# Performance work log

Measured on AMD Instinct MI355X. Metric: run time of the kernel, lower is better.

Reference implementation:

```python
import jax, jax.numpy as jnp
import numpy as np

B, S, D, H = 32, 8192, 256, 256


def setup_inputs() -> dict:
    key = jax.random.key(0)
    ks = jax.random.split(key, 8)
    # start token: module uses np.random.seed(42); np.random.random([B,1,D])
    rng = np.random.RandomState(42)
    start_token = jnp.asarray(rng.random_sample((B, 1, D)).astype(np.float32))
    s = 0.05  # weight init scale
    return {
        "encoder_output": jax.random.normal(ks[0], (B, S, D), jnp.float32),
        "h0": jax.random.normal(ks[1], (B, H), jnp.float32),
        "c0": jax.random.normal(ks[2], (B, H), jnp.float32),
        "start_token": start_token,
        # Keras LSTM params: kernel [D,4H], recurrent_kernel [H,4H], bias [4H]; gate order i,f,c,o
        "W_k": jax.random.normal(ks[3], (D, 4 * H), jnp.float32) * s,
        "W_r": jax.random.normal(ks[4], (H, 4 * H), jnp.float32) * s,
        "b_lstm": jnp.zeros((4 * H,), jnp.float32),
        # encoder_weight Dense(H), decode_weight Dense(H), v Dense(1)
        "W_e": jax.random.normal(ks[5], (D, H), jnp.float32) * s,
        "b_e": jnp.zeros((H,), jnp.float32),
        "W_d": jax.random.normal(ks[6], (H, H), jnp.float32) * s,
        "b_d": jnp.zeros((H,), jnp.float32),
        "v_w": jax.random.normal(ks[7], (H, 1), jnp.float32) * s,
        "v_b": jnp.zeros((1,), jnp.float32),
    }


def reference(encoder_output, h0, c0, start_token, W_k, W_r, b_lstm,
              W_e, b_e, W_d, b_d, v_w, v_b):
    # --- one Keras-LSTM step on the start token (seq_len = 1) ---
    x = start_token[:, 0, :]                      # [B, D]
    z = x @ W_k + h0 @ W_r + b_lstm               # [B, 4H]
    i, f, g, o = jnp.split(z, 4, axis=-1)         # Keras gate order i,f,c,o
    c = jax.nn.sigmoid(f) * c0 + jax.nn.sigmoid(i) * jnp.tanh(g)
    h = jax.nn.sigmoid(o) * jnp.tanh(c)           # [B, H] decoder output
    # --- Bahdanau additive attention (vectorized form of the double loop) ---
    dec_proj = h @ W_d + b_d                      # [B, H]
    enc_proj = encoder_output @ W_e + b_e         # [B, S, H]
    # tanh(enc_proj + dec_proj) projected to scalar by v
    scores = jnp.tanh(enc_proj + dec_proj[:, None, :]) @ v_w  # [B, S, 1]
    scores = scores[..., 0] + v_b                 # [B, S]
    return jax.nn.softmax(scores, axis=-1)
```

## Files before the change

kernel.cpp:

```cpp
#include <hip/hip_runtime.h>
#include <hip/hip_bf16.h>
#include <stdint.h>

#define B 32
#define S 8192
#define D 256
#define H 256

typedef __attribute__((ext_vector_type(8))) short bf16x8;
typedef __attribute__((ext_vector_type(4))) float f32x4;

#define GLOBAL_AS __attribute__((address_space(1)))
#define LDS_AS __attribute__((address_space(3)))

__device__ inline unsigned short f2bf(float f) {
  unsigned u = __float_as_uint(f);
  unsigned r = (u + 0x7FFFu + ((u >> 16) & 1u)) >> 16;
  return (unsigned short)r;
}

__device__ inline unsigned pk2bf(float a, float b) {
  __hip_bfloat162 h = __float22bfloat162_rn(make_float2(a, b));
  unsigned u;
  __builtin_memcpy(&u, &h, 4);
  return u;
}

__device__ inline bf16x8 pack8(float4 a, float4 b) {
  union { unsigned u[4]; bf16x8 v; } c;
  c.u[0] = pk2bf(a.x, a.y);
  c.u[1] = pk2bf(a.z, a.w);
  c.u[2] = pk2bf(b.x, b.y);
  c.u[3] = pk2bf(b.z, b.w);
  return c.v;
}

__device__ inline float fast_tanh(float x) {
  float e = __expf(2.0f * x);
  return 1.0f - 2.0f * __builtin_amdgcn_rcpf(1.0f + e);
}

__global__ __launch_bounds__(1024) void prep_kernel(
    const float* __restrict__ h0, const float* __restrict__ c0,
    const float* __restrict__ start_token, const float* __restrict__ W_k,
    const float* __restrict__ W_r, const float* __restrict__ b_lstm,
    const float* __restrict__ W_e, const float* __restrict__ W_d,
    const float* __restrict__ b_d, const float* __restrict__ b_e,
    unsigned short* __restrict__ Wfrag, float* __restrict__ decb) {
  int blk = blockIdx.x;
  int tid = threadIdx.x;

  __shared__ float xs[D], hs[H], zs[4 * H], hv[H], dpp[4][H];

  if (blk < 64) {
    int gid = blk * 1024 + tid;
    int j = gid & 7;
    int lane = (gid >> 3) & 63;
    int kt = (gid >> 9) & 7;
    int nt = gid >> 12;
    int n = nt * 16 + (lane & 15);
    int k = kt * 32 + (lane >> 4) * 8 + j;
    Wfrag[gid] = f2bf(W_e[k * H + n]);
  } else {
    int b = blk - 64;
    if (tid < D) xs[tid] = start_token[b * D + tid];
    else if (tid < 2 * D) hs[tid - D] = h0[b * H + (tid - D)];
    __syncthreads();
    {
      int jj = tid;
      float a0 = 0.f, a1 = 0.f, a2 = 0.f, a3 = 0.f;
      #pragma unroll 8
      for (int d = 0; d < D; d += 4) {
        a0 += xs[d + 0] * W_k[(d + 0) * 1024 + jj];
        a1 += xs[d + 1] * W_k[(d + 1) * 1024 + jj];
        a2 += xs[d + 2] * W_k[(d + 2) * 1024 + jj];
        a3 += xs[d + 3] * W_k[(d + 3) * 1024 + jj];
      }
      #pragma unroll 8
      for (int h = 0; h < H; h += 4) {
        a0 += hs[h + 0] * W_r[(h + 0) * 1024 + jj];
        a1 += hs[h + 1] * W_r[(h + 1) * 1024 + jj];
        a2 += hs[h + 2] * W_r[(h + 2) * 1024 + jj];
        a3 += hs[h + 3] * W_r[(h + 3) * 1024 + jj];
      }
      zs[jj] = b_lstm[jj] + ((a0 + a1) + (a2 + a3));
    }
    __syncthreads();
    if (tid < H) {
      float zi = zs[tid], zf = zs[H + tid], zg = zs[2 * H + tid], zo = zs[3 * H + tid];
      float si = 1.0f / (1.0f + expf(-zi));
      float sf = 1.0f / (1.0f + expf(-zf));
      float so = 1.0f / (1.0f + expf(-zo));
      float c = sf * c0[b * H + tid] + si * tanhf(zg);
      hv[tid] = so * tanhf(c);
    }
    __syncthreads();
    {
      int hcol = tid & (H - 1);
      int q = tid >> 8;
      float a = 0.f;
      #pragma unroll 8
      for (int k = q * 64; k < q * 64 + 64; ++k) a += hv[k] * W_d[k * H + hcol];
      dpp[q][hcol] = a;
    }
    __syncthreads();
    if (tid < H)
      decb[b * H + tid] = dpp[0][tid] + dpp[1][tid] + dpp[2][tid] + dpp[3][tid]
                        + b_d[tid] + b_e[tid];
  }
}

__global__ __launch_bounds__(256, 2) void attn_kernel(
    const float* __restrict__ enc, const unsigned short* __restrict__ Wfrag,
    const float* __restrict__ decb, const float* __restrict__ v_w,
    float* __restrict__ scores4) {
  __shared__ float Abuf[2][32 * 256];

  const int tid = threadIdx.x;
  const int wave = tid >> 6, lane = tid & 63;
  const int ml = lane & 15, kg = lane >> 4;
  const int bid = blockIdx.x;
  const int batch = bid >> 4;
  const long row_blk = (long)bid * 512;

  bf16x8 wfr[4][8];
  #pragma unroll
  for (int q = 0; q < 4; ++q)
    #pragma unroll
    for (int kt = 0; kt < 8; ++kt)
      wfr[q][kt] = *(const bf16x8*)(Wfrag + ((size_t)(((wave * 4 + q) * 8 + kt) * 64 + lane) << 3));

  float bs[4], vw[4];
  #pragma unroll
  for (int q = 0; q < 4; ++q) {
    int n = wave * 64 + q * 16 + ml;
    bs[q] = decb[batch * 256 + n];
    vw[q] = v_w[n];
  }

  auto stage = [&](int t, int sel) {
    const float* gtile = enc + (row_blk + (long)t * 32) * D;
    #pragma unroll
    for (int is = 0; is < 8; ++is) {
      int row = is * 4 + wave;
      int c = lane ^ (row & 7);
      const float* gp = gtile + row * D + c * 4;
      float* lp = &Abuf[sel][(is * 256 + wave * 64) * 4];
      __builtin_amdgcn_global_load_lds((const GLOBAL_AS void*)gp,
                                       (LDS_AS void*)lp, 16, 0, 0);
    }
  };

  stage(0, 0);

  #pragma unroll 2
  for (int t = 0; t < 16; ++t) {
    __syncthreads();
    if (t + 1 < 16) stage(t + 1, (t + 1) & 1);

    const float* Ab = Abuf[t & 1];
    f32x4 acc[2][4];
    #pragma unroll
    for (int i = 0; i < 2; ++i)
      #pragma unroll
      for (int q = 0; q < 4; ++q) acc[i][q] = (f32x4){0.f, 0.f, 0.f, 0.f};

    #pragma unroll
    for (int kt = 0; kt < 8; ++kt) {
      #pragma unroll
      for (int i = 0; i < 2; ++i) {
        int row = i * 16 + ml;
        int x = ml & 7;
        int c0 = kt * 8 + kg * 2;
        float4 v0 = *(const float4*)&Ab[(row * 64 + (c0 ^ x)) * 4];
        float4 v1 = *(const float4*)&Ab[(row * 64 + ((c0 + 1) ^ x)) * 4];
        bf16x8 af = pack8(v0, v1);
        #pragma unroll
        for (int q = 0; q < 4; ++q)
          acc[i][q] = __builtin_amdgcn_mfma_f32_16x16x32_bf16(af, wfr[q][kt], acc[i][q], 0, 0, 0);
      }
    }

    float part[8];
    #pragma unroll
    for (int v = 0; v < 8; ++v) part[v] = 0.f;
    #pragma unroll
    for (int q = 0; q < 4; ++q)
      #pragma unroll
      for (int i = 0; i < 2; ++i)
        #pragma unroll
        for (int r = 0; r < 4; ++r)
          part[i * 4 + r] += fast_tanh(acc[i][q][r] + bs[q]) * vw[q];
    #pragma unroll
    for (int m = 1; m < 16; m <<= 1)
      #pragma unroll
      for (int v = 0; v < 8; ++v) part[v] += __shfl_xor(part[v], m, 64);
    if (ml == 0) {
      long r0 = row_blk + (long)t * 32 + kg * 4;
      #pragma unroll
      for (int i = 0; i < 2; ++i)
        #pragma unroll
        for (int r = 0; r < 4; ++r)
          scores4[(r0 + i * 16 + r) * 4 + wave] = part[i * 4 + r];
    }
  }
}

__global__ __launch_bounds__(1024) void softmax_kernel(
    const float* __restrict__ scores4, float* __restrict__ out) {
  int b = blockIdx.x;
  int tid = threadIdx.x;
  __shared__ float red[16];
  const float* src = scores4 + (long)b * S * 4;
  float v[8];
  float lmax = -1e30f;
  #pragma unroll
  for (int j = 0; j < 8; ++j) {
    float4 t4 = *(const float4*)(src + (size_t)(tid + j * 1024) * 4);
    v[j] = (t4.x + t4.y) + (t4.z + t4.w);
    lmax = fmaxf(lmax, v[j]);
  }
  #pragma unroll
  for (int m = 1; m < 64; m <<= 1) lmax = fmaxf(lmax, __shfl_xor(lmax, m, 64));
  if ((tid & 63) == 0) red[tid >> 6] = lmax;
  __syncthreads();
  float M = red[0];
  #pragma unroll
  for (int i = 1; i < 16; ++i) M = fmaxf(M, red[i]);
  __syncthreads();
  float ls = 0.f;
  #pragma unroll
  for (int j = 0; j < 8; ++j) {
    v[j] = __expf(v[j] - M);
    ls += v[j];
  }
  #pragma unroll
  for (int m = 1; m < 64; m <<= 1) ls += __shfl_xor(ls, m, 64);
  if ((tid & 63) == 0) red[tid >> 6] = ls;
  __syncthreads();
  float total = 0.f;
  #pragma unroll
  for (int i = 0; i < 16; ++i) total += red[i];
  float inv = __builtin_amdgcn_rcpf(total);
  #pragma unroll
  for (int j = 0; j < 8; ++j) out[(long)b * S + tid + j * 1024] = v[j] * inv;
}

extern "C" void kernel_launch(void* const* d_in, const int* in_sizes, int n_in,
                              void* d_out, int out_size, void* d_ws, size_t ws_size,
                              hipStream_t stream) {
  const float* enc         = (const float*)d_in[0];
  const float* h0          = (const float*)d_in[1];
  const float* c0          = (const float*)d_in[2];
  const float* start_token = (const float*)d_in[3];
  const float* W_k         = (const float*)d_in[4];
  const float* W_r         = (const float*)d_in[5];
  const float* b_lstm      = (const float*)d_in[6];
  const float* W_e         = (const float*)d_in[7];
  const float* b_e         = (const float*)d_in[8];
  const float* W_d         = (const float*)d_in[9];
  const float* b_d         = (const float*)d_in[10];
  const float* v_w         = (const float*)d_in[11];
  float* out = (float*)d_out;

  char* wsb = (char*)d_ws;
  float* scores4        = (float*)wsb;
  unsigned short* Wfrag = (unsigned short*)(wsb + (size_t)B * S * 16);
  float* decb           = (float*)(wsb + (size_t)B * S * 16 + (size_t)D * H * 2);

  prep_kernel<<<96, 1024, 0, stream>>>(h0, c0, start_token, W_k, W_r, b_lstm,
                                       W_e, W_d, b_d, b_e, Wfrag, decb);
  attn_kernel<<<512, 256, 0, stream>>>(enc, Wfrag, decb, v_w, scores4);
  softmax_kernel<<<B, 1024, 0, stream>>>(scores4, out);
}
```

Before: 433.8 us.

## Load encoder tiles directly into registers instead of LDS double buffering

```diff
diff --git a/kernel.cpp b/kernel.cpp
--- a/kernel.cpp
+++ b/kernel.cpp
@@ -9,9 +9,6 @@
 
 typedef __attribute__((ext_vector_type(8))) short bf16x8;
 typedef __attribute__((ext_vector_type(4))) float f32x4;
-
-#define GLOBAL_AS __attribute__((address_space(1)))
-#define LDS_AS __attribute__((address_space(3)))
 
 __device__ inline unsigned short f2bf(float f) {
   unsigned u = __float_as_uint(f);
@@ -110,18 +107,16 @@
   }
 }
 
-__global__ __launch_bounds__(256, 2) void attn_kernel(
+__global__ __launch_bounds__(256, 1) void attn_kernel(
     const float* __restrict__ enc, const unsigned short* __restrict__ Wfrag,
     const float* __restrict__ decb, const float* __restrict__ v_w,
     float* __restrict__ scores4) {
-  __shared__ float Abuf[2][32 * 256];
-
   const int tid = threadIdx.x;
   const int wave = tid >> 6, lane = tid & 63;
   const int ml = lane & 15, kg = lane >> 4;
   const int bid = blockIdx.x;
-  const int batch = bid >> 4;
-  const long row_blk = (long)bid * 512;
+  const int batch = bid >> 6;
+  const long row_blk = (long)bid * 128;
 
   bf16x8 wfr[4][8];
   #pragma unroll
@@ -138,27 +133,19 @@
     vw[q] = v_w[n];
   }
 
-  auto stage = [&](int t, int sel) {
-    const float* gtile = enc + (row_blk + (long)t * 32) * D;
-    #pragma unroll
-    for (int is = 0; is < 8; ++is) {
-      int row = is * 4 + wave;
-      int c = lane ^ (row & 7);
-      const float* gp = gtile + row * D + c * 4;
-      float* lp = &Abuf[sel][(is * 256 + wave * 64) * 4];
-      __builtin_amdgcn_global_load_lds((const GLOBAL_AS void*)gp,
-                                       (LDS_AS void*)lp, 16, 0, 0);
-    }
-  };
-
-  stage(0, 0);
-
-  #pragma unroll 2
-  for (int t = 0; t < 16; ++t) {
-    __syncthreads();
-    if (t + 1 < 16) stage(t + 1, (t + 1) & 1);
-
-    const float* Ab = Abuf[t & 1];
+  for (int t = 0; t < 4; ++t) {
+    const float* arow0 = enc + (row_blk + t * 32 + ml) * (long)D + kg * 8;
+    const float* arow1 = arow0 + 16 * D;
+
+    float4 a[8][2][2];
+    #pragma unroll
+    for (int kt = 0; kt < 8; ++kt) {
+      a[kt][0][0] = *(const float4*)(arow0 + kt * 32);
+      a[kt][0][1] = *(const float4*)(arow0 + kt * 32 + 4);
+      a[kt][1][0] = *(const float4*)(arow1 + kt * 32);
+      a[kt][1][1] = *(const float4*)(arow1 + kt * 32 + 4);
+    }
+
     f32x4 acc[2][4];
     #pragma unroll
     for (int i = 0; i < 2; ++i)
@@ -167,17 +154,12 @@
 
     #pragma unroll
     for (int kt = 0; kt < 8; ++kt) {
-      #pragma unroll
-      for (int i = 0; i < 2; ++i) {
-        int row = i * 16 + ml;
-        int x = ml & 7;
-        int c0 = kt * 8 + kg * 2;
-        float4 v0 = *(const float4*)&Ab[(row * 64 + (c0 ^ x)) * 4];
-        float4 v1 = *(const float4*)&Ab[(row * 64 + ((c0 + 1) ^ x)) * 4];
-        bf16x8 af = pack8(v0, v1);
-        #pragma unroll
-        for (int q = 0; q < 4; ++q)
-          acc[i][q] = __builtin_amdgcn_mfma_f32_16x16x32_bf16(af, wfr[q][kt], acc[i][q], 0, 0, 0);
+      bf16x8 af0 = pack8(a[kt][0][0], a[kt][0][1]);
+      bf16x8 af1 = pack8(a[kt][1][0], a[kt][1][1]);
+      #pragma unroll
+      for (int q = 0; q < 4; ++q) {
+        acc[0][q] = __builtin_amdgcn_mfma_f32_16x16x32_bf16(af0, wfr[q][kt], acc[0][q], 0, 0, 0);
+        acc[1][q] = __builtin_amdgcn_mfma_f32_16x16x32_bf16(af1, wfr[q][kt], acc[1][q], 0, 0, 0);
       }
     }
 
@@ -196,7 +178,7 @@
       #pragma unroll
       for (int v = 0; v < 8; ++v) part[v] += __shfl_xor(part[v], m, 64);
     if (ml == 0) {
-      long r0 = row_blk + (long)t * 32 + kg * 4;
+      long r0 = row_blk + t * 32 + kg * 4;
       #pragma unroll
       for (int i = 0; i < 2; ++i)
         #pragma unroll
@@ -270,6 +252,6 @@
 
   prep_kernel<<<96, 1024, 0, stream>>>(h0, c0, start_token, W_k, W_r, b_lstm,
                                        W_e, W_d, b_d, b_e, Wfrag, decb);
-  attn_kernel<<<512, 256, 0, stream>>>(enc, Wfrag, decb, v_w, scores4);
+  attn_kernel<<<2048, 256, 0, stream>>>(enc, Wfrag, decb, v_w, scores4);
   softmax_kernel<<<B, 1024, 0, stream>>>(scores4, out);
 }
```

Result: slower. 486.8 us (+12.2%).
